# Kernel optimization log

Measured on AMD Instinct MI355X. Metric: run time of the kernel, lower is better.

## Reference

```python
import jax, jax.numpy as jnp
import numpy as np

H = 256  # hidden size


def _gru_layer(x_seq, W_ih, W_hh, b_ih, b_hh):
    # x_seq: (S, B, D_in). PyTorch gate order: r, z, n.
    S, B = x_seq.shape[0], x_seq.shape[1]
    x_proj = jnp.einsum('sbd,gd->sbg', x_seq, W_ih) + b_ih  # (S, B, 3H)
    h0 = jnp.zeros((B, H), dtype=x_seq.dtype)

    def step(h, xp):
        gh = h @ W_hh.T + b_hh  # (B, 3H)
        xr, xz, xn = xp[:, :H], xp[:, H:2 * H], xp[:, 2 * H:]
        hr, hz, hn = gh[:, :H], gh[:, H:2 * H], gh[:, 2 * H:]
        r = jax.nn.sigmoid(xr + hr)
        z = jax.nn.sigmoid(xz + hz)
        n = jnp.tanh(xn + r * hn)
        h_new = (1.0 - z) * n + z * h
        return h_new, h_new

    hT, ys = jax.lax.scan(step, h0, x_proj)
    return ys, hT  # ys: (S, B, H), hT: (B, H)


def setup_inputs() -> dict:
    key = jax.random.key(0)
    ks = jax.random.split(key, 11)
    S, B, D, O = 2048, 256, 64, 32
    s_ih0 = 1.0 / np.sqrt(H)
    inp = {
        'x': jax.random.normal(ks[0], (S, B, D), dtype=jnp.float32),
        'W_ih0': jax.random.normal(ks[1], (3 * H, D), dtype=jnp.float32) * s_ih0,
        'W_hh0': jax.random.normal(ks[2], (3 * H, H), dtype=jnp.float32) * s_ih0,
        'b_ih0': jax.random.normal(ks[3], (3 * H,), dtype=jnp.float32) * s_ih0,
        'b_hh0': jax.random.normal(ks[4], (3 * H,), dtype=jnp.float32) * s_ih0,
        'W_ih1': jax.random.normal(ks[5], (3 * H, H), dtype=jnp.float32) * s_ih0,
        'W_hh1': jax.random.normal(ks[6], (3 * H, H), dtype=jnp.float32) * s_ih0,
        'b_ih1': jax.random.normal(ks[7], (3 * H,), dtype=jnp.float32) * s_ih0,
        'b_hh1': jax.random.normal(ks[8], (3 * H,), dtype=jnp.float32) * s_ih0,
        'W_out': jax.random.normal(ks[9], (O, H), dtype=jnp.float32) * s_ih0,
        'b_out': jax.random.normal(ks[10], (O,), dtype=jnp.float32) * s_ih0,
    }
    return inp


def reference(x, W_ih0, W_hh0, b_ih0, b_hh0, W_ih1, W_hh1, b_ih1, b_hh1, W_out, b_out):
    ys0, h0T = _gru_layer(x, W_ih0, W_hh0, b_ih0, b_hh0)
    ys1, h1T = _gru_layer(ys0, W_ih1, W_hh1, b_ih1, b_hh1)
    hn = jnp.stack([h0T, h1T], axis=0)  # (n_layers, B, H)
    out = jnp.tanh(hn @ W_out.T + b_out)  # (n_layers, B, O)
    return out
```

## Files before the change

### kernel.cpp

```cpp
#include <hip/hip_runtime.h>
#include <stdint.h>

#define HH 256
#define SS 2048
#define BB 256
#define DD 64
#define CHS 32
#define RING 8

typedef __attribute__((ext_vector_type(8))) short bh8;
typedef __attribute__((ext_vector_type(4))) float fx4;
typedef __attribute__((ext_vector_type(4))) float f4v;

#define L0TAG_OFF 0ull
#define L1TAG_OFF 2048ull
#define P0TAG_OFF 4096ull
#define P1TAG_OFF 8192ull
#define BF0_OFF   12288ull
#define BF1_OFF   16384ull
#define FIN_OFF   20480ull
#define WBF0_OFF  524288ull
#define WBF1_OFF  1048576ull
#define YS_OFF    2097152ull
#define XP0_OFF   37748736ull
#define XP1_OFF   139460608ull
#define WS_NEED   (XP1_OFF + 100663296ull)

__device__ __forceinline__ short f2bf(float f) {
  uint32_t u = __builtin_bit_cast(uint32_t, f);
  u += 0x7FFFu + ((u >> 16) & 1u);
  return (short)(u >> 16);
}
__device__ __forceinline__ float bf2f(short s) {
  uint32_t u = ((uint32_t)(uint16_t)s) << 16;
  return __builtin_bit_cast(float, u);
}
__device__ __forceinline__ float lof(int u) {
  return __builtin_bit_cast(float, (uint32_t)u << 16);
}
__device__ __forceinline__ float hif(int u) {
  return __builtin_bit_cast(float, (uint32_t)u & 0xFFFF0000u);
}
__device__ __forceinline__ uint32_t pack2(float a, float b) {
  return ((uint32_t)(uint16_t)f2bf(a)) | (((uint32_t)(uint16_t)f2bf(b)) << 16);
}
__device__ __forceinline__ float rcp_(float x) { return __builtin_amdgcn_rcpf(x); }
__device__ __forceinline__ float tanh_(float x) {
  x = fminf(fmaxf(x, -15.f), 15.f);
  float e = __expf(2.0f * x);
  return (e - 1.0f) / (e + 1.0f);
}
__device__ __forceinline__ fx4 mfma16(bh8 a, bh8 b, fx4 c) {
  return __builtin_amdgcn_mfma_f32_16x16x32_bf16(a, b, c, 0, 0, 0);
}
__device__ __forceinline__ bh8 cvt8(f4v a, f4v b) {
  bh8 r;
  r[0]=f2bf(a[0]); r[1]=f2bf(a[1]); r[2]=f2bf(a[2]); r[3]=f2bf(a[3]);
  r[4]=f2bf(b[0]); r[5]=f2bf(b[1]); r[6]=f2bf(b[2]); r[7]=f2bf(b[3]);
  return r;
}
__device__ __forceinline__ bh8 gld16_cc(const short* p) {
  bh8 r; asm volatile("global_load_dwordx4 %0, %1, off sc0 sc1" : "=v"(r) : "v"(p));
  return r;
}
__device__ __forceinline__ void stw_cc(uint32_t* p, uint32_t v) {
  asm volatile("global_store_dword %0, %1, off sc0 sc1" :: "v"(p), "v"(v) : "memory");
}
__device__ __forceinline__ void vwait0() {
  asm volatile("s_waitcnt vmcnt(0)" ::: "memory");
  __builtin_amdgcn_sched_barrier(0);
}
__device__ __forceinline__ void vwait1() {
  asm volatile("s_waitcnt vmcnt(1)" ::: "memory");
  __builtin_amdgcn_sched_barrier(0);
}
template<int SLP>
__device__ __forceinline__ void wait_nz_cc(const uint32_t* p) {
  for (;;) {
    uint32_t v;
    asm volatile("global_load_dword %0, %1, off sc0 sc1" : "=v"(v) : "v"(p));
    asm volatile("s_waitcnt vmcnt(0)" ::: "memory");
    if (v != 0u) break;
    __builtin_amdgcn_s_sleep(SLP);
  }
  __builtin_amdgcn_sched_barrier(0);
}
template<int SLP>
__device__ __forceinline__ void wait_ge_cc(const uint32_t* p, uint32_t need) {
  for (;;) {
    uint32_t v;
    asm volatile("global_load_dword %0, %1, off sc0 sc1" : "=v"(v) : "v"(p));
    asm volatile("s_waitcnt vmcnt(0)" ::: "memory");
    if (v >= need) break;
    __builtin_amdgcn_s_sleep(SLP);
  }
  __builtin_amdgcn_sched_barrier(0);
}

#define ISSUE_XP(T) \
  { const short* b_ = xp + ((size_t)(((((T) >> 5) & 7))*16 + g)*32 + ((T) & 31))*12288 + w*1536 + l*4; \
    asm volatile("global_load_dwordx2 %0, %1, off sc0 sc1"             : "=v"(xA) : "v"(b_)); \
    asm volatile("global_load_dwordx2 %0, %1, off offset:512 sc0 sc1"  : "=v"(xB) : "v"(b_)); \
    asm volatile("global_load_dwordx2 %0, %1, off offset:1024 sc0 sc1" : "=v"(xC) : "v"(b_)); \
    asm volatile("global_load_dwordx2 %0, %1, off offset:1536 sc0 sc1" : "=v"(xD) : "v"(b_)); \
    asm volatile("global_load_dwordx2 %0, %1, off offset:2048 sc0 sc1" : "=v"(xE) : "v"(b_)); \
    asm volatile("global_load_dwordx2 %0, %1, off offset:2560 sc0 sc1" : "=v"(xF) : "v"(b_)); }

#define CTL_BODY(CTL, PR, PZ, PN, BHN)                                           \
  {                                                                              \
    fx4 accR, accZ, accN;                                                        \
    accR[0]=lof(PR.x); accR[1]=hif(PR.x); accR[2]=lof(PR.y); accR[3]=hif(PR.y);  \
    accZ[0]=lof(PZ.x); accZ[1]=hif(PZ.x); accZ[2]=lof(PZ.y); accZ[3]=hif(PZ.y);  \
    float xn0=lof(PN.x), xn1=hif(PN.x), xn2=lof(PN.y), xn3=hif(PN.y);            \
    accN[0]=0.f; accN[1]=0.f; accN[2]=0.f; accN[3]=0.f;                          \
    _Pragma("unroll")                                                            \
    for (int kf = 0; kf < 8; ++kf) {                                             \
      bh8 a = *(const bh8*)&pubp[rb + kf*512 + l*8];                             \
      accR = mfma16(a, whhF[CTL][0][kf], accR);                                  \
      accZ = mfma16(a, whhF[CTL][1][kf], accZ);                                  \
      accN = mfma16(a, whhF[CTL][2][kf], accN);                                  \
    }                                                                            \
    _Pragma("unroll")                                                            \
    for (int i = 0; i < 4; ++i) {                                                \
      float xnv = (i==0)?xn0:((i==1)?xn1:((i==2)?xn2:xn3));                      \
      float r = rcp_(1.0f + __expf(-accR[i]));                                   \
      float z = rcp_(1.0f + __expf(-accZ[i]));                                   \
      float na = xnv + r * (accN[i] + (BHN));                                    \
      float n = 1.0f - 2.0f * rcp_(__expf(2.0f*na) + 1.0f);                      \
      float h = n + z * (hp[(CTL)*4+i] - n);                                     \
      hp[(CTL)*4+i] = h;                                                         \
      int la = lg*4 + i + 16*((CTL)*2 + b3);                                     \
      pubp[wb + la*8 + j7] = f2bf(h);                                            \
    }                                                                            \
  }

template<int LAYER>
__device__ __forceinline__ void run_rec(
    const float* __restrict__ Whh, const float* __restrict__ bhh,
    uint8_t* __restrict__ ws, int g, short* pubp)
{
  const int tid = threadIdx.x;
  const int w = tid >> 6, l = tid & 63;
  const int l15 = l & 15, lg = l >> 4;
  const int b3 = l15 >> 3, j7 = l & 7;

  for (int i = tid; i < 8192; i += 512) pubp[i] = 0;

  bh8 whhF[2][3][8];
#pragma unroll
  for (int ctl = 0; ctl < 2; ++ctl) {
    const int col = (2*w + ctl)*16 + l15;
#pragma unroll
    for (int gate = 0; gate < 3; ++gate) {
      const float* base = Whh + (size_t)(gate*HH + col)*HH;
#pragma unroll
      for (int kf = 0; kf < 8; ++kf) {
        const float* p = base + kf*32 + lg*8;
        whhF[ctl][gate][kf] = cvt8(*(const f4v*)p, *(const f4v*)(p + 4));
      }
    }
  }
#pragma unroll
  for (int ctl = 0; ctl < 2; ++ctl)
#pragma unroll
    for (int gate = 0; gate < 3; ++gate)
#pragma unroll
      for (int kf = 0; kf < 8; ++kf)
        asm volatile("" : "+v"(whhF[ctl][gate][kf]));

  const float bhN0 = bhh[2*HH + (2*w + 0)*16 + l15];
  const float bhN1 = bhh[2*HH + (2*w + 1)*16 + l15];

  uint32_t* mytag       = (uint32_t*)(ws + (LAYER ? L1TAG_OFF : L0TAG_OFF) + (size_t)g*128);
  const uint32_t* ptag  = (const uint32_t*)(ws + (LAYER ? P1TAG_OFF : P0TAG_OFF)) + g*64;
  const uint32_t* bptag = (const uint32_t*)(ws + P1TAG_OFF) + g*64;
  short* xp  = (short*)(ws + (LAYER ? XP1_OFF : XP0_OFF));
  short* ys  = (short*)(ws + YS_OFF);
  short* fin = (short*)(ws + FIN_OFF);

  __syncthreads();

  wait_nz_cc<1>(ptag);
  int2 xA, xB, xC, xD, xE, xF;
  ISSUE_XP(0);
  float hp[8] = {0,0,0,0,0,0,0,0};

  for (int t = 0; t < SS; ++t) {
    const int buf = t & 1;
    const int rb = (buf ^ 1)*4096;
    const int wb = buf*4096 + w*512;
    if (LAYER == 0 && (t & (CHS-1)) != 0) vwait1(); else vwait0();

    CTL_BODY(0, xA, xB, xC, bhN0)
    CTL_BODY(1, xD, xE, xF, bhN1)

    const int tn = t + 1;
    if (tn < SS) {
      if ((tn & (CHS-1)) == 0) {
        wait_nz_cc<2>(ptag + (tn >> 5));
        if (LAYER == 0 && (tn >> 5) >= RING) wait_nz_cc<2>(bptag + ((tn >> 5) - RING));
      }
      ISSUE_XP(tn);
    }
    if (LAYER == 0) {
      bh8 mf = *(const bh8*)&pubp[buf*4096 + w*512 + l*8];
      short* dst = ys + ((size_t)(((t >> 5) & 7)*16 + g)*32 + (t & 31))*4096 + w*512 + l*8;
      asm volatile("global_store_dwordx4 %0, %1, off sc0 sc1" :: "v"(dst), "v"(mf) : "memory");
    }
    __syncthreads();
    if ((tn & (CHS-1)) == 0) {
      asm volatile("s_waitcnt vmcnt(0)" ::: "memory");
      __syncthreads();
      if (tid == 0) stw_cc(mytag, (uint32_t)tn);
    }
  }
  bh8 mf = *(const bh8*)&pubp[4096 + w*512 + l*8];
  short* dst = fin + ((size_t)(LAYER*16 + g)*8 + w)*512 + l*8;
  asm volatile("global_store_dwordx4 %0, %1, off sc0 sc1" :: "v"(dst), "v"(mf) : "memory");
  asm volatile("s_waitcnt vmcnt(0)" ::: "memory");
}

__device__ __forceinline__ void run_proj0(const float* __restrict__ x,
                                          uint8_t* __restrict__ ws, int g, int c)
{
  const int tid = threadIdx.x, w = tid >> 6, l = tid & 63, l15 = l & 15, lg = l >> 4;
  if (c >= RING)
    wait_ge_cc<3>((const uint32_t*)(ws + L0TAG_OFF + (size_t)g*128), (uint32_t)(CHS*(c - RING + 1)));
  bh8 A[4][2];
#pragma unroll
  for (int tt = 0; tt < 4; ++tt) {
    const int t = c*32 + w*4 + tt;
#pragma unroll
    for (int kf = 0; kf < 2; ++kf) {
      const float* p = x + ((size_t)t*BB + g*16 + l15)*DD + kf*32 + lg*8;
      A[tt][kf] = cvt8(*(const f4v*)p, *(const f4v*)(p + 4));
    }
  }
  const bh8* WB = (const bh8*)(ws + WBF0_OFF);
  const float* BF = (const float*)(ws + BF0_OFF);
  short* xp0 = (short*)(ws + XP0_OFF);
  const size_t obase = ((size_t)((c & 7)*16 + g)*32 + w*4)*12288 + l*4;
  for (int ct = 0; ct < 48; ++ct) {
    bh8 B0 = WB[(size_t)(ct*2 + 0)*64 + l];
    bh8 B1 = WB[(size_t)(ct*2 + 1)*64 + l];
    const float bb = BF[(ct >> 4)*256 + (ct & 15)*16 + l15];
    const int fid = (ct & 15)*3 + (ct >> 4);
#pragma unroll
    for (int tt = 0; tt < 4; ++tt) {
      fx4 acc = {0.f, 0.f, 0.f, 0.f};
      acc = mfma16(A[tt][0], B0, acc);
      acc = mfma16(A[tt][1], B1, acc);
      int2 v;
      v.x = (int)pack2(acc[0] + bb, acc[1] + bb);
      v.y = (int)pack2(acc[2] + bb, acc[3] + bb);
      short* dst = xp0 + obase + (size_t)tt*12288 + fid*256;
      asm volatile("global_store_dwordx2 %0, %1, off sc0 sc1" :: "v"(dst), "v"(v) : "memory");
    }
  }
  asm volatile("s_waitcnt vmcnt(0)" ::: "memory");
  __syncthreads();
  if (tid == 0) stw_cc((uint32_t*)(ws + P0TAG_OFF) + g*64 + c, 1u);
}

__device__ __forceinline__ void run_proj1(uint8_t* __restrict__ ws, int g, int c)
{
  const int tid = threadIdx.x, w = tid >> 6, l = tid & 63, l15 = l & 15;
  wait_ge_cc<3>((const uint32_t*)(ws + L0TAG_OFF + (size_t)g*128), (uint32_t)(CHS*(c + 1)));
  if (c >= RING)
    wait_ge_cc<3>((const uint32_t*)(ws + L1TAG_OFF + (size_t)g*128), (uint32_t)(CHS*(c - RING + 1)));
  const short* ys = (const short*)(ws + YS_OFF) + ((size_t)((c & 7)*16 + g)*32)*4096;
  bh8 A[4][8];
#pragma unroll
  for (int tt = 0; tt < 4; ++tt)
#pragma unroll
    for (int kf = 0; kf < 8; ++kf)
      A[tt][kf] = gld16_cc(ys + (size_t)(w*4 + tt)*4096 + kf*512 + l*8);
  asm volatile("s_waitcnt vmcnt(0)" ::: "memory");
  __builtin_amdgcn_sched_barrier(0);
  const bh8* WB = (const bh8*)(ws + WBF1_OFF);
  const float* BF = (const float*)(ws + BF1_OFF);
  short* xp1 = (short*)(ws + XP1_OFF);
  const size_t obase = ((size_t)((c & 7)*16 + g)*32 + w*4)*12288 + l*4;
  for (int ct = 0; ct < 48; ++ct) {
    bh8 B[8];
#pragma unroll
    for (int kf = 0; kf < 8; ++kf) B[kf] = WB[(size_t)(ct*8 + kf)*64 + l];
    const float bb = BF[(ct >> 4)*256 + (ct & 15)*16 + l15];
    const int fid = (ct & 15)*3 + (ct >> 4);
#pragma unroll
    for (int tt = 0; tt < 4; ++tt) {
      fx4 acc = {0.f, 0.f, 0.f, 0.f};
#pragma unroll
      for (int kf = 0; kf < 8; ++kf) acc = mfma16(A[tt][kf], B[kf], acc);
      int2 v;
      v.x = (int)pack2(acc[0] + bb, acc[1] + bb);
      v.y = (int)pack2(acc[2] + bb, acc[3] + bb);
      short* dst = xp1 + obase + (size_t)tt*12288 + fid*256;
      asm volatile("global_store_dwordx2 %0, %1, off sc0 sc1" :: "v"(dst), "v"(v) : "memory");
    }
  }
  asm volatile("s_waitcnt vmcnt(0)" ::: "memory");
  __syncthreads();
  if (tid == 0) stw_cc((uint32_t*)(ws + P1TAG_OFF) + g*64 + c, 1u);
}

__global__ __launch_bounds__(512) void gru_prep(
    const float* __restrict__ Wih0, const float* __restrict__ Wih1,
    const float* __restrict__ bih0, const float* __restrict__ bhh0,
    const float* __restrict__ bih1, const float* __restrict__ bhh1,
    uint8_t* __restrict__ ws)
{
  const int bid = blockIdx.x, tid = threadIdx.x;
  if (bid == 60) {
    float* BF0 = (float*)(ws + BF0_OFF);
    float* BF1 = (float*)(ws + BF1_OFF);
    for (int i = tid; i < 768; i += 512) {
      const int gate = i >> 8;
      BF0[i] = bih0[i] + (gate < 2 ? bhh0[i] : 0.f);
      BF1[i] = bih1[i] + (gate < 2 ? bhh1[i] : 0.f);
    }
    return;
  }
  const int W = bid*8 + (tid >> 6), l = tid & 63, l15 = l & 15, lg = l >> 4;
  if (W < 96) {
    const int ct = W >> 1, kf = W & 1;
    const float* p = Wih0 + (size_t)(ct*16 + l15)*DD + kf*32 + lg*8;
    ((bh8*)(ws + WBF0_OFF))[(size_t)W*64 + l] = cvt8(*(const f4v*)p, *(const f4v*)(p + 4));
  } else {
    const int V = W - 96, ct = V >> 3, kf = V & 7;
    const float* p = Wih1 + (size_t)(ct*16 + l15)*HH + kf*32 + lg*8;
    ((bh8*)(ws + WBF1_OFF))[(size_t)V*64 + l] = cvt8(*(const f4v*)p, *(const f4v*)(p + 4));
  }
}

__global__ __launch_bounds__(512)
__attribute__((amdgpu_waves_per_eu(2, 2)))
void gru_mega(
    const float* __restrict__ x,
    const float* __restrict__ Whh0, const float* __restrict__ bhh0,
    const float* __restrict__ Whh1, const float* __restrict__ bhh1,
    uint8_t* __restrict__ ws)
{
  __shared__ short pubp[8192];
  const int bid = blockIdx.x;
  if (bid < 16)      run_rec<0>(Whh0, bhh0, ws, bid, pubp);
  else if (bid < 32) run_rec<1>(Whh1, bhh1, ws, bid - 16, pubp);
  else {
    const int j = bid - 32, c = j >> 5, r = j & 31;
    if (r < 16) run_proj0(x, ws, r, c);
    else        run_proj1(ws, r - 16, c);
  }
}

__global__ __launch_bounds__(512) void gru_out(
    const uint8_t* __restrict__ ws,
    const float* __restrict__ Wout, const float* __restrict__ bout,
    float* __restrict__ out)
{
  const short* fin = (const short*)(ws + FIN_OFF);
  const int bid = blockIdx.x;
  const int layer = bid >> 4, g = bid & 15;
  const int tid = threadIdx.x;
  const int row = tid >> 5, o = tid & 31;
  const short* src = fin + (size_t)(layer*16 + g)*4096;
  float acc = 0.f;
#pragma unroll 8
  for (int h = 0; h < HH; ++h) {
    const int f = h >> 5, lane = row + ((h & 31) >> 3)*16, idx = h & 7;
    acc += bf2f(src[f*512 + lane*8 + idx]) * Wout[o*HH + h];
  }
  out[((size_t)(layer*BB) + g*16 + row)*32 + o] = tanh_(acc + bout[o]);
}

extern "C" void kernel_launch(void* const* d_in, const int* in_sizes, int n_in,
                              void* d_out, int out_size, void* d_ws, size_t ws_size,
                              hipStream_t stream) {
  const float* x    = (const float*)d_in[0];
  const float* Wih0 = (const float*)d_in[1];
  const float* Whh0 = (const float*)d_in[2];
  const float* bih0 = (const float*)d_in[3];
  const float* bhh0 = (const float*)d_in[4];
  const float* Wih1 = (const float*)d_in[5];
  const float* Whh1 = (const float*)d_in[6];
  const float* bih1 = (const float*)d_in[7];
  const float* bhh1 = (const float*)d_in[8];
  const float* Wout = (const float*)d_in[9];
  const float* bout = (const float*)d_in[10];
  uint8_t* ws = (uint8_t*)d_ws;

  if (ws_size < WS_NEED) return;

  (void)hipMemsetAsync(ws, 0, 16384, stream);
  gru_prep<<<dim3(61), dim3(512), 0, stream>>>(Wih0, Wih1, bih0, bhh0, bih1, bhh1, ws);
  gru_mega<<<dim3(2080), dim3(512), 0, stream>>>(x, Whh0, bhh0, Whh1, bhh1, ws);
  gru_out<<<dim3(32), dim3(512), 0, stream>>>(ws, Wout, bout, (float*)d_out);
}
```

Before: 3.589 ms.

## Double-buffer x-projection loads two steps ahead in GRU recurrence loop

Unrolls the recurrent loop by two and keeps two register sets of x-projection values, issuing the loads for step t+2 so global-load latency is hidden across a full step. It also hoists the eight LDS reads of the hidden state into an array shared by both column tiles instead of reloading them per tile. The cost is more live registers, and a full vmcnt(0) wait on even steps that also drains the previous step's ys stores.

```diff
diff --git a/kernel.cpp b/kernel.cpp
--- a/kernel.cpp
+++ b/kernel.cpp
@@ -70,10 +70,6 @@
   asm volatile("s_waitcnt vmcnt(0)" ::: "memory");
   __builtin_amdgcn_sched_barrier(0);
 }
-__device__ __forceinline__ void vwait1() {
-  asm volatile("s_waitcnt vmcnt(1)" ::: "memory");
-  __builtin_amdgcn_sched_barrier(0);
-}
 template<int SLP>
 __device__ __forceinline__ void wait_nz_cc(const uint32_t* p) {
   for (;;) {
@@ -97,41 +93,85 @@
   __builtin_amdgcn_sched_barrier(0);
 }
 
-#define ISSUE_XP(T) \
+#define ISSUE_XP(T, rA,rB,rC,rD,rE,rF) \
   { const short* b_ = xp + ((size_t)(((((T) >> 5) & 7))*16 + g)*32 + ((T) & 31))*12288 + w*1536 + l*4; \
-    asm volatile("global_load_dwordx2 %0, %1, off sc0 sc1"             : "=v"(xA) : "v"(b_)); \
-    asm volatile("global_load_dwordx2 %0, %1, off offset:512 sc0 sc1"  : "=v"(xB) : "v"(b_)); \
-    asm volatile("global_load_dwordx2 %0, %1, off offset:1024 sc0 sc1" : "=v"(xC) : "v"(b_)); \
-    asm volatile("global_load_dwordx2 %0, %1, off offset:1536 sc0 sc1" : "=v"(xD) : "v"(b_)); \
-    asm volatile("global_load_dwordx2 %0, %1, off offset:2048 sc0 sc1" : "=v"(xE) : "v"(b_)); \
-    asm volatile("global_load_dwordx2 %0, %1, off offset:2560 sc0 sc1" : "=v"(xF) : "v"(b_)); }
-
-#define CTL_BODY(CTL, PR, PZ, PN, BHN)                                           \
-  {                                                                              \
-    fx4 accR, accZ, accN;                                                        \
-    accR[0]=lof(PR.x); accR[1]=hif(PR.x); accR[2]=lof(PR.y); accR[3]=hif(PR.y);  \
-    accZ[0]=lof(PZ.x); accZ[1]=hif(PZ.x); accZ[2]=lof(PZ.y); accZ[3]=hif(PZ.y);  \
-    float xn0=lof(PN.x), xn1=hif(PN.x), xn2=lof(PN.y), xn3=hif(PN.y);            \
-    accN[0]=0.f; accN[1]=0.f; accN[2]=0.f; accN[3]=0.f;                          \
-    _Pragma("unroll")                                                            \
-    for (int kf = 0; kf < 8; ++kf) {                                             \
-      bh8 a = *(const bh8*)&pubp[rb + kf*512 + l*8];                             \
-      accR = mfma16(a, whhF[CTL][0][kf], accR);                                  \
-      accZ = mfma16(a, whhF[CTL][1][kf], accZ);                                  \
-      accN = mfma16(a, whhF[CTL][2][kf], accN);                                  \
-    }                                                                            \
-    _Pragma("unroll")                                                            \
-    for (int i = 0; i < 4; ++i) {                                                \
-      float xnv = (i==0)?xn0:((i==1)?xn1:((i==2)?xn2:xn3));                      \
-      float r = rcp_(1.0f + __expf(-accR[i]));                                   \
-      float z = rcp_(1.0f + __expf(-accZ[i]));                                   \
-      float na = xnv + r * (accN[i] + (BHN));                                    \
-      float n = 1.0f - 2.0f * rcp_(__expf(2.0f*na) + 1.0f);                      \
-      float h = n + z * (hp[(CTL)*4+i] - n);                                     \
-      hp[(CTL)*4+i] = h;                                                         \
-      int la = lg*4 + i + 16*((CTL)*2 + b3);                                     \
-      pubp[wb + la*8 + j7] = f2bf(h);                                            \
-    }                                                                            \
+    asm volatile("global_load_dwordx2 %0, %1, off sc0 sc1"             : "=v"(rA) : "v"(b_)); \
+    asm volatile("global_load_dwordx2 %0, %1, off offset:512 sc0 sc1"  : "=v"(rB) : "v"(b_)); \
+    asm volatile("global_load_dwordx2 %0, %1, off offset:1024 sc0 sc1" : "=v"(rC) : "v"(b_)); \
+    asm volatile("global_load_dwordx2 %0, %1, off offset:1536 sc0 sc1" : "=v"(rD) : "v"(b_)); \
+    asm volatile("global_load_dwordx2 %0, %1, off offset:2048 sc0 sc1" : "=v"(rE) : "v"(b_)); \
+    asm volatile("global_load_dwordx2 %0, %1, off offset:2560 sc0 sc1" : "=v"(rF) : "v"(b_)); }
+
+#define CTL_MFMA(CTL, accR, accZ, accN) \
+  _Pragma("unroll") \
+  for (int kf = 0; kf < 8; ++kf) { \
+    accR = mfma16(af[kf], whhF[CTL][0][kf], accR); \
+    accZ = mfma16(af[kf], whhF[CTL][1][kf], accZ); \
+    accN = mfma16(af[kf], whhF[CTL][2][kf], accN); \
+  }
+
+#define CTL_GATES(CTL, accR, accZ, accN, X0,X1,X2,X3, BHN) \
+  _Pragma("unroll") \
+  for (int i = 0; i < 4; ++i) { \
+    float xnv = (i==0)?(X0):((i==1)?(X1):((i==2)?(X2):(X3))); \
+    float r = rcp_(1.0f + __expf(-accR[i])); \
+    float z = rcp_(1.0f + __expf(-accZ[i])); \
+    float na = xnv + r * (accN[i] + (BHN)); \
+    float n = 1.0f - 2.0f * rcp_(__expf(2.0f*na) + 1.0f); \
+    float h = n + z * (hp[(CTL)*4+i] - n); \
+    hp[(CTL)*4+i] = h; \
+    int la = lg*4 + i + 16*((CTL)*2 + b3); \
+    pubp[wb + la*8 + j7] = f2bf(h); \
+  }
+
+#define REC_STEP2(T, rA,rB,rC,rD,rE,rF, ISEVEN) \
+  { \
+    if (ISEVEN) { \
+      asm volatile("s_waitcnt vmcnt(0)" ::: "memory"); \
+      __builtin_amdgcn_sched_barrier(0); \
+    } \
+    const int t_ = (T); \
+    const int buf = t_ & 1; \
+    const int rb = (buf ^ 1) * 4096; \
+    const int wb = buf * 4096 + w * 512; \
+    fx4 aR0, aZ0, aR1, aZ1; \
+    fx4 aN0 = {0.f,0.f,0.f,0.f}, aN1 = {0.f,0.f,0.f,0.f}; \
+    aR0[0]=lof(rA.x); aR0[1]=hif(rA.x); aR0[2]=lof(rA.y); aR0[3]=hif(rA.y); \
+    aZ0[0]=lof(rB.x); aZ0[1]=hif(rB.x); aZ0[2]=lof(rB.y); aZ0[3]=hif(rB.y); \
+    float x0=lof(rC.x), x1=hif(rC.x), x2=lof(rC.y), x3=hif(rC.y); \
+    aR1[0]=lof(rD.x); aR1[1]=hif(rD.x); aR1[2]=lof(rD.y); aR1[3]=hif(rD.y); \
+    aZ1[0]=lof(rE.x); aZ1[1]=hif(rE.x); aZ1[2]=lof(rE.y); aZ1[3]=hif(rE.y); \
+    float x4=lof(rF.x), x5=hif(rF.x), x6=lof(rF.y), x7=hif(rF.y); \
+    const int tn2_ = t_ + 2; \
+    if (tn2_ < SS) { \
+      if (ISEVEN && (tn2_ & (CHS-1)) == 0) { \
+        wait_nz_cc<2>(ptag + (tn2_ >> 5)); \
+        if (LAYER == 0 && (tn2_ >> 5) >= RING) \
+          wait_nz_cc<2>(bptag + ((tn2_ >> 5) - RING)); \
+      } \
+      ISSUE_XP(tn2_, rA,rB,rC,rD,rE,rF); \
+    } \
+    bh8 af[8]; \
+    _Pragma("unroll") \
+    for (int kf = 0; kf < 8; ++kf) af[kf] = *(const bh8*)&pubp[rb + kf*512 + l*8]; \
+    CTL_MFMA(0, aR0, aZ0, aN0) \
+    CTL_GATES(0, aR0, aZ0, aN0, x0,x1,x2,x3, bhN0) \
+    CTL_MFMA(1, aR1, aZ1, aN1) \
+    CTL_GATES(1, aR1, aZ1, aN1, x4,x5,x6,x7, bhN1) \
+    if (LAYER == 0) { \
+      bh8 mf = *(const bh8*)&pubp[wb + l*8]; \
+      short* dst = ys + ((size_t)(((t_ >> 5) & 7)*16 + g)*32 + (t_ & 31))*4096 + w*512 + l*8; \
+      asm volatile("global_store_dwordx4 %0, %1, off sc0 sc1" :: "v"(dst), "v"(mf) : "memory"); \
+    } \
+    __syncthreads(); \
+    if (!ISEVEN) { \
+      const int tn_ = t_ + 1; \
+      if ((tn_ & (CHS-1)) == 0) { \
+        asm volatile("s_waitcnt vmcnt(0)" ::: "memory"); \
+        __syncthreads(); \
+        if (tid == 0) stw_cc(mytag, (uint32_t)tn_); \
+      } \
+    } \
   }
 
 template<int LAYER>
@@ -181,39 +221,17 @@
   __syncthreads();
 
   wait_nz_cc<1>(ptag);
-  int2 xA, xB, xC, xD, xE, xF;
-  ISSUE_XP(0);
+  int2 xA0,xB0,xC0,xD0,xE0,xF0, xA1,xB1,xC1,xD1,xE1,xF1;
+  ISSUE_XP(0, xA0,xB0,xC0,xD0,xE0,xF0);
+  ISSUE_XP(1, xA1,xB1,xC1,xD1,xE1,xF1);
+
   float hp[8] = {0,0,0,0,0,0,0,0};
 
-  for (int t = 0; t < SS; ++t) {
-    const int buf = t & 1;
-    const int rb = (buf ^ 1)*4096;
-    const int wb = buf*4096 + w*512;
-    if (LAYER == 0 && (t & (CHS-1)) != 0) vwait1(); else vwait0();
-
-    CTL_BODY(0, xA, xB, xC, bhN0)
-    CTL_BODY(1, xD, xE, xF, bhN1)
-
-    const int tn = t + 1;
-    if (tn < SS) {
-      if ((tn & (CHS-1)) == 0) {
-        wait_nz_cc<2>(ptag + (tn >> 5));
-        if (LAYER == 0 && (tn >> 5) >= RING) wait_nz_cc<2>(bptag + ((tn >> 5) - RING));
-      }
-      ISSUE_XP(tn);
-    }
-    if (LAYER == 0) {
-      bh8 mf = *(const bh8*)&pubp[buf*4096 + w*512 + l*8];
-      short* dst = ys + ((size_t)(((t >> 5) & 7)*16 + g)*32 + (t & 31))*4096 + w*512 + l*8;
-      asm volatile("global_store_dwordx4 %0, %1, off sc0 sc1" :: "v"(dst), "v"(mf) : "memory");
-    }
-    __syncthreads();
-    if ((tn & (CHS-1)) == 0) {
-      asm volatile("s_waitcnt vmcnt(0)" ::: "memory");
-      __syncthreads();
-      if (tid == 0) stw_cc(mytag, (uint32_t)tn);
-    }
-  }
+  for (int tp = 0; tp < SS; tp += 2) {
+    REC_STEP2(tp,     xA0,xB0,xC0,xD0,xE0,xF0, 1)
+    REC_STEP2(tp + 1, xA1,xB1,xC1,xD1,xE1,xF1, 0)
+  }
+
   bh8 mf = *(const bh8*)&pubp[4096 + w*512 + l*8];
   short* dst = fin + ((size_t)(LAYER*16 + g)*8 + w)*512 + l*8;
   asm volatile("global_store_dwordx4 %0, %1, off sc0 sc1" :: "v"(dst), "v"(mf) : "memory");
```

Result: slower. 6.711 ms (+87.0%).
